# Performance work log

Measured on AMD Instinct MI355X. Metric: run time of the kernel, lower is better.

## Reference

```python
import jax, jax.numpy as jnp
import numpy as np

NUM_HEADS = 16
ROPE_BASE = 10000.0


def _rope(x):
    """Standard rotary embedding. x: (B, H, T, Dh), positions 0..T-1."""
    T, Dh = x.shape[-2], x.shape[-1]
    half = Dh // 2
    inv_freq = 1.0 / (ROPE_BASE ** (jnp.arange(half, dtype=jnp.float32) / half))
    ang = jnp.arange(T, dtype=jnp.float32)[:, None] * inv_freq[None, :]  # (T, half)
    cos, sin = jnp.cos(ang), jnp.sin(ang)
    x1, x2 = x[..., :half], x[..., half:]
    return jnp.concatenate([x1 * cos - x2 * sin, x1 * sin + x2 * cos], axis=-1)


def setup_inputs() -> dict:
    key = jax.random.key(0)
    ks = jax.random.split(key, 5)
    B, N, D = 8, 1025, 1024
    s = 1.0 / np.sqrt(D)
    return {
        "x": jax.random.normal(ks[0], (B, N, D), jnp.float32),
        "wq": jax.random.normal(ks[1], (D, D), jnp.float32) * s,
        "wk": jax.random.normal(ks[2], (D, D), jnp.float32) * s,
        "wv": jax.random.normal(ks[3], (D, D), jnp.float32) * s,
        "q_bias": jnp.zeros((D,), jnp.float32),
        "v_bias": jnp.zeros((D,), jnp.float32),
        "w_out": jax.random.normal(ks[4], (D, D), jnp.float32) * s,
        "b_out": jnp.zeros((D,), jnp.float32),
    }


def reference(x, wq, wk, wv, q_bias, v_bias, w_out, b_out):
    B, N, D = x.shape
    H = NUM_HEADS
    Dh = D // H
    scale = Dh ** -0.5

    q = x @ wq + q_bias           # (B, N, D)
    k = x @ wk
    v = x @ wv + v_bias

    def split_heads(t):  # (B, N, D) -> (B, H, N, Dh)
        return t.reshape(B, N, H, Dh).transpose(0, 2, 1, 3)

    q, k, v = split_heads(q), split_heads(k), split_heads(v)

    # RoPE on all tokens except the first (CLS)
    q = jnp.concatenate([q[:, :, :1, :], _rope(q[:, :, 1:, :])], axis=2)
    k = jnp.concatenate([k[:, :, :1, :], _rope(k[:, :, 1:, :])], axis=2)

    attn = jnp.einsum('bhqd,bhkd->bhqk', q * scale, k)
    attn = jax.nn.softmax(attn, axis=-1)
    out = jnp.einsum('bhqk,bhkd->bhqd', attn, v)  # (B, H, N, Dh)
    out = out.transpose(0, 2, 1, 3).reshape(B, N, D)
    return out @ w_out + b_out
```

## Files before the change

kernel.cpp:

```cpp
#include <hip/hip_runtime.h>

typedef unsigned short u16;
typedef __attribute__((ext_vector_type(8))) short  short8;
typedef __attribute__((ext_vector_type(8))) __bf16 bf16x8;
typedef __attribute__((ext_vector_type(4))) __bf16 bf16x4;
typedef __attribute__((ext_vector_type(4))) float  f32x4;

#define DEV __device__ __forceinline__

#define BATCH 8
#define SEQ   1025
#define DMODEL 1024
#define NHEAD 16
#define DH    64
#define MROWS (BATCH*SEQ)
#define VPAD  1152
#define KROWS 1088

DEV float bf2f(u16 u) { union { unsigned int i; float f; } v; v.i = ((unsigned int)u) << 16; return v.f; }
DEV u16 f2bf(float f) {
  union { float f; unsigned int i; } v; v.f = f;
  unsigned int x = v.i;
  return (u16)((x + 0x7fffu + ((x >> 16) & 1u)) >> 16);
}

DEV f32x4 mfma16(bf16x8 a, bf16x8 b, f32x4 c) {
  return __builtin_amdgcn_mfma_f32_16x16x32_bf16(a, b, c, 0, 0, 0);
}

DEV void gload_lds16(const void* g, void* s) {
  __builtin_amdgcn_global_load_lds(
      (const __attribute__((address_space(1))) void*)g,
      (__attribute__((address_space(3))) void*)s, 16, 0, 0);
}

DEV float exp2_fast(float x) { float r; asm("v_exp_f32 %0, %1" : "=v"(r) : "v"(x)); return r; }
DEV unsigned cvt_pk_bf16(float lo, float hi) {
  unsigned r;
  asm("v_cvt_pk_bf16_f32 %0, %1, %2" : "=v"(r) : "v"(lo), "v"(hi));
  return r;
}

#define QSCALE (0.125f * 1.44269504088896341f)

__global__ void prep_kernel(const float* __restrict__ x,
                            const float* __restrict__ wq, const float* __restrict__ wk,
                            const float* __restrict__ wv, const float* __restrict__ wo,
                            u16* __restrict__ x_bf, u16* __restrict__ wtqkv,
                            u16* __restrict__ wtout,
                            float* __restrict__ cost, float* __restrict__ sint) {
  __shared__ float tile[64][65];
  const int blk = blockIdx.x, tid = threadIdx.x;
  if (blk < 4100) {
    int i = blk * 256 + tid;
    if (i >= MROWS * 1024 / 8) return;
    const float4* p = (const float4*)x + (size_t)i * 2;
    float4 a = p[0], b = p[1];
    short8 o;
    o[0] = (short)f2bf(a.x); o[1] = (short)f2bf(a.y); o[2] = (short)f2bf(a.z); o[3] = (short)f2bf(a.w);
    o[4] = (short)f2bf(b.x); o[5] = (short)f2bf(b.y); o[6] = (short)f2bf(b.z); o[7] = (short)f2bf(b.w);
    *(short8*)(x_bf + (size_t)i * 8) = o;
  } else if (blk < 5124) {
    int wg = blk - 4100;
    int z = wg >> 8, rem = wg & 255;
    int kx = rem & 15, ny = rem >> 4;
    const float* src = (z == 0) ? wq : (z == 1) ? wk : (z == 2) ? wv : wo;
    int k0 = kx * 64, n0 = ny * 64;
    int c = tid & 63, rq = tid >> 6;
#pragma unroll
    for (int p = 0; p < 16; ++p) {
      int r = p * 4 + rq;
      tile[r][c] = src[(size_t)(k0 + r) * 1024 + n0 + c];
    }
    __syncthreads();
    u16* dst = (z < 3) ? (wtqkv + (size_t)z * 1024 * 1024) : wtout;
#pragma unroll
    for (int p = 0; p < 16; ++p) {
      int r = p * 4 + rq;
      dst[(size_t)(n0 + r) * 1024 + k0 + c] = f2bf(tile[c][r]);
    }
  } else {
    int i = (blk - 5124) * 256 + tid;
    if (i >= 1024 * 32) return;
    int pos = i >> 5, d = i & 31;
    float inv = powf(10000.0f, -(float)d / 32.0f);
    float ang = (float)pos * inv;
    cost[i] = cosf(ang);
    sint[i] = sinf(ang);
  }
}

#define FENCE(N) asm volatile("s_waitcnt vmcnt(" N ") lgkmcnt(0)\n\ts_barrier" ::: "memory")

DEV void stage_half(const u16* __restrict__ gpanel, long row0, int kcol,
                    char* dst, int wid, int lane) {
#pragma unroll
  for (int s = 0; s < 2; ++s) {
    int tt = wid * 64 + lane;
    int row = s * 128 + (tt >> 2), c2 = tt & 3;
    const u16* src = gpanel + (row0 + row) * 1024 + kcol + ((c2 ^ ((row >> 1) & 3)) << 3);
    gload_lds16(src, dst + s * 8192 + wid * 1024);
  }
}

DEV void quad(const char* sm, int buf, int kk, int mh, int wrow, int wcol,
              int l4, int l15, f32x4 (&acc)[8][4]) {
  const char* Ab = sm + buf * 65536 + kk * 16384;
  const char* Bb = sm + buf * 65536 + 32768 + kk * 16384;
  bf16x8 bfr[4];
#pragma unroll
  for (int n = 0; n < 4; ++n) {
    int r = wcol * 64 + n * 16 + l15;
    bfr[n] = *(const bf16x8*)(Bb + r * 64 + ((l4 << 4) ^ (((r >> 1) & 3) << 4)));
  }
  bf16x8 af[4];
#pragma unroll
  for (int m = 0; m < 4; ++m) {
    int r = wrow * 128 + (mh * 4 + m) * 16 + l15;
    af[m] = *(const bf16x8*)(Ab + r * 64 + ((l4 << 4) ^ (((r >> 1) & 3) << 4)));
  }
  __builtin_amdgcn_s_setprio(1);
#pragma unroll
  for (int m = 0; m < 4; ++m)
#pragma unroll
    for (int n = 0; n < 4; ++n)
      acc[mh * 4 + m][n] = mfma16(af[m], bfr[n], acc[mh * 4 + m][n]);
  __builtin_amdgcn_s_setprio(0);
}

__global__ __launch_bounds__(512, 2) void gemm256(const u16* __restrict__ A,
    const u16* __restrict__ Bw, u16* __restrict__ Cout) {
  __shared__ char smem[131072];
  int mt, nt;
  {
    int orig = blockIdx.x;
    int xcd = orig & 7;
    int f = (xcd < 4 ? xcd * 50 : 200 + (xcd - 4) * 49) + (orig >> 3);
    if (f < 384) { int sr = f / 48, rem = f % 48; nt = rem >> 2; mt = sr * 4 + (rem & 3); }
    else { mt = 32; nt = f - 384; }
  }
  const int t = threadIdx.x;
  const int wid = t >> 6, lane = t & 63;
  const int l4 = lane >> 4, l15 = lane & 15;
  const int wrow = wid >> 2, wcol = wid & 3;
  const long rowA0 = (long)mt * 256;
  const long rowB0 = (long)nt * 256;

  f32x4 acc[8][4];
#pragma unroll
  for (int m = 0; m < 8; ++m)
#pragma unroll
    for (int n = 0; n < 4; ++n) { f32x4 z = {0.f,0.f,0.f,0.f}; acc[m][n] = z; }

  stage_half(A,  rowA0, 0,  smem + 0,     wid, lane);
  stage_half(Bw, rowB0, 0,  smem + 32768, wid, lane);
  stage_half(A,  rowA0, 32, smem + 16384, wid, lane);
  stage_half(Bw, rowB0, 32, smem + 49152, wid, lane);

  for (int j = 0; j < 7; ++j) {
    const int cY = (2 * j + 1) * 64, cX = (2 * j + 2) * 64;
    FENCE("4"); stage_half(A,  rowA0, cY,      smem + 65536 + 0,     wid, lane); quad(smem, 0, 0, 0, wrow, wcol, l4, l15, acc);
    FENCE("6"); stage_half(Bw, rowB0, cY,      smem + 65536 + 32768, wid, lane); quad(smem, 0, 0, 1, wrow, wcol, l4, l15, acc);
    FENCE("4"); stage_half(A,  rowA0, cY + 32, smem + 65536 + 16384, wid, lane); quad(smem, 0, 1, 0, wrow, wcol, l4, l15, acc);
    FENCE("6"); stage_half(Bw, rowB0, cY + 32, smem + 65536 + 49152, wid, lane); quad(smem, 0, 1, 1, wrow, wcol, l4, l15, acc);
    FENCE("4"); stage_half(A,  rowA0, cX,      smem + 0,     wid, lane); quad(smem, 1, 0, 0, wrow, wcol, l4, l15, acc);
    FENCE("6"); stage_half(Bw, rowB0, cX,      smem + 32768, wid, lane); quad(smem, 1, 0, 1, wrow, wcol, l4, l15, acc);
    FENCE("4"); stage_half(A,  rowA0, cX + 32, smem + 16384, wid, lane); quad(smem, 1, 1, 0, wrow, wcol, l4, l15, acc);
    FENCE("6"); stage_half(Bw, rowB0, cX + 32, smem + 49152, wid, lane); quad(smem, 1, 1, 1, wrow, wcol, l4, l15, acc);
  }
  {
    const int cY = 15 * 64;
    FENCE("4"); stage_half(A,  rowA0, cY,      smem + 65536 + 0,     wid, lane); quad(smem, 0, 0, 0, wrow, wcol, l4, l15, acc);
    FENCE("6"); stage_half(Bw, rowB0, cY,      smem + 65536 + 32768, wid, lane); quad(smem, 0, 0, 1, wrow, wcol, l4, l15, acc);
    FENCE("4"); stage_half(A,  rowA0, cY + 32, smem + 65536 + 16384, wid, lane); quad(smem, 0, 1, 0, wrow, wcol, l4, l15, acc);
    FENCE("6"); stage_half(Bw, rowB0, cY + 32, smem + 65536 + 49152, wid, lane); quad(smem, 0, 1, 1, wrow, wcol, l4, l15, acc);
    FENCE("4"); quad(smem, 1, 0, 0, wrow, wcol, l4, l15, acc);
    FENCE("4"); quad(smem, 1, 0, 1, wrow, wcol, l4, l15, acc);
    FENCE("0"); quad(smem, 1, 1, 0, wrow, wcol, l4, l15, acc);
    FENCE("0"); quad(smem, 1, 1, 1, wrow, wcol, l4, l15, acc);
  }

#pragma unroll
  for (int m = 0; m < 8; ++m)
#pragma unroll
    for (int rg = 0; rg < 4; ++rg) {
      long row = rowA0 + wrow * 128 + m * 16 + l4 * 4 + rg;
      if (row >= MROWS) continue;
#pragma unroll
      for (int n = 0; n < 4; ++n) {
        long col = rowB0 + wcol * 64 + n * 16 + l15;
        Cout[row * 3072 + col] = f2bf(acc[m][n][rg]);
      }
    }
}

DEV void map_tiles(int f, int MT, int NT, int& mt, int& nt) {
  int body = (MT & ~7) * NT;
  if (f >= body) { int r = f - body; mt = (MT & ~7) + r / NT; nt = r % NT; }
  else { int sr = f / (8 * NT); int rem = f - sr * 8 * NT; nt = rem >> 3; mt = sr * 8 + (rem & 7); }
}

__global__ __launch_bounds__(256) void gemm_out(const u16* __restrict__ A,
    const u16* __restrict__ Bw, float* __restrict__ Cout, const float* __restrict__ bias) {
  __shared__ char smem[32768];
  int mt, nt;
  { int wg = blockIdx.x; int f = (wg & 7) * 65 + (wg >> 3); map_tiles(f, 65, 8, mt, nt); }
  const int t = threadIdx.x;
  const int wid = t >> 6, lane = t & 63;
  const int l4 = lane >> 4, l15 = lane & 15;
  const int wr = wid >> 1, wc = wid & 1;
  const long rowA0 = (long)mt * 128;
  const long rowB0 = (long)nt * 128;

  f32x4 acc[4][4];
#pragma unroll
  for (int m = 0; m < 4; ++m)
#pragma unroll
    for (int n = 0; n < 4; ++n) { f32x4 z = {0.f,0.f,0.f,0.f}; acc[m][n] = z; }

  const int srow = t >> 3;
  const int scol = (t & 7) * 8;

  for (int k0 = 0; k0 < 1024; k0 += 64) {
    __syncthreads();
#pragma unroll
    for (int i = 0; i < 4; ++i) {
      const u16* ga = A  + (rowA0 + i * 32 + srow) * 1024 + k0 + scol;
      gload_lds16(ga, smem + i * 4096 + wid * 1024);
      const u16* gb = Bw + (rowB0 + i * 32 + srow) * 1024 + k0 + scol;
      gload_lds16(gb, smem + 16384 + i * 4096 + wid * 1024);
    }
    __syncthreads();

    bf16x8 af[4][2], bfr[4][2];
#pragma unroll
    for (int m = 0; m < 4; ++m)
#pragma unroll
      for (int kk = 0; kk < 2; ++kk)
        af[m][kk] = *(const bf16x8*)(smem + (wr * 64 + m * 16 + l15) * 128 + kk * 64 + l4 * 16);
#pragma unroll
    for (int n = 0; n < 4; ++n)
#pragma unroll
      for (int kk = 0; kk < 2; ++kk)
        bfr[n][kk] = *(const bf16x8*)(smem + 16384 + (wc * 64 + n * 16 + l15) * 128 + kk * 64 + l4 * 16);

#pragma unroll
    for (int m = 0; m < 4; ++m)
#pragma unroll
      for (int n = 0; n < 4; ++n)
#pragma unroll
        for (int kk = 0; kk < 2; ++kk)
          acc[m][n] = mfma16(af[m][kk], bfr[n][kk], acc[m][n]);
  }

#pragma unroll
  for (int m = 0; m < 4; ++m)
#pragma unroll
    for (int rg = 0; rg < 4; ++rg) {
      long row = rowA0 + wr * 64 + m * 16 + l4 * 4 + rg;
      if (row >= MROWS) continue;
#pragma unroll
      for (int n = 0; n < 4; ++n) {
        long col = rowB0 + wc * 64 + n * 16 + l15;
        Cout[row * 1024 + col] = acc[m][n][rg] + bias[col];
      }
    }
}

__global__ void postqkv_kernel(const u16* __restrict__ cq, const float* __restrict__ qb,
                               const float* __restrict__ vb,
                               const float* __restrict__ cost, const float* __restrict__ sint,
                               u16* __restrict__ Qh, u16* __restrict__ Kh,
                               u16* __restrict__ VTh) {
  __shared__ float tile[64][65];
  const int blk = blockIdx.x, tid = threadIdx.x;
  if (blk < 513) {
    int idx = blk * 256 + tid;
    if (idx >= MROWS * NHEAD) return;
    int h = idx & 15, row = idx >> 4;
    int b = row / SEQ, n = row - b * SEQ;
    const u16* src = cq + (size_t)row * 3072 + h * 64;
    size_t dq = ((size_t)(b * 16 + h) * SEQ   + n) * 64;
    size_t dk = ((size_t)(b * 16 + h) * KROWS + n) * 64;
    bool dorope = (n > 0);
    const float* ct = cost + (size_t)(n - 1) * 32;
    const float* st = sint + (size_t)(n - 1) * 32;
#pragma unroll
    for (int i = 0; i < 4; ++i) {
      short8 qlo = *(const short8*)(src + i * 8);
      short8 qhi = *(const short8*)(src + 32 + i * 8);
      short8 klo = *(const short8*)(src + 1024 + i * 8);
      short8 khi = *(const short8*)(src + 1024 + 32 + i * 8);
      short8 oqlo, oqhi, oklo, okhi;
#pragma unroll
      for (int j = 0; j < 8; ++j) {
        int d = i * 8 + j;
        float q1 = bf2f((u16)qlo[j]) + qb[h * 64 + d];
        float q2 = bf2f((u16)qhi[j]) + qb[h * 64 + 32 + d];
        float k1 = bf2f((u16)klo[j]);
        float k2 = bf2f((u16)khi[j]);
        float c = dorope ? ct[d] : 1.0f;
        float s = dorope ? st[d] : 0.0f;
        oqlo[j] = (short)f2bf((q1 * c - q2 * s) * QSCALE);
        oqhi[j] = (short)f2bf((q1 * s + q2 * c) * QSCALE);
        oklo[j] = (short)f2bf(k1 * c - k2 * s);
        okhi[j] = (short)f2bf(k1 * s + k2 * c);
      }
      *(short8*)(Qh + dq + i * 8)      = oqlo;
      *(short8*)(Qh + dq + 32 + i * 8) = oqhi;
      *(short8*)(Kh + dk + i * 8)      = oklo;
      *(short8*)(Kh + dk + 32 + i * 8) = okhi;
    }
  } else {
    int wg = blk - 513;
    int bh = wg / 18, nx = wg - bh * 18;
    int b = bh >> 4, h = bh & 15;
    int n0 = nx * 64;
    int c = tid & 63, rq = tid >> 6;
#pragma unroll
    for (int p = 0; p < 16; ++p) {
      int r = p * 4 + rq;
      int n = n0 + r;
      float v = 0.f;
      if (n < SEQ) v = bf2f(cq[(size_t)(b * SEQ + n) * 3072 + 2048 + h * 64 + c]) + vb[h * 64 + c];
      tile[r][c] = v;
    }
    __syncthreads();
#pragma unroll
    for (int p = 0; p < 16; ++p) {
      int d = p * 4 + rq;
      VTh[((size_t)bh * 64 + d) * VPAD + n0 + c] = f2bf(tile[c][d]);
    }
  }
}

DEV void stage_rows(const u16* __restrict__ g, size_t strideElems, char* lbase,
                    int wid, int lane) {
#pragma unroll
  for (int s = 0; s < 2; ++s) {
    int off = s * 4096 + wid * 1024 + lane * 16;
    int r = off >> 7, cs = (off >> 4) & 7;
    const u16* src = g + (size_t)r * strideElems + ((cs ^ (r & 7)) << 3);
    gload_lds16(src, lbase + s * 4096 + wid * 1024);
  }
}

__global__ __launch_bounds__(256, 4) void attn128(const u16* __restrict__ Qh,
    const u16* __restrict__ Kh, const u16* __restrict__ VTh,
    u16* __restrict__ xattn) {
  __shared__ char lds[32768];
  const int wg = blockIdx.x;
  const int x = (wg & 7) * 144 + (wg >> 3);
  const int qt = x % 9, bh = x / 9;
  const int b = bh >> 4, h = bh & 15;
  const int t = threadIdx.x, w = t >> 6, lane = t & 63;
  const int l4 = lane >> 4, l15 = lane & 15;
  const u16* Qb = Qh + (size_t)bh * (SEQ * 64);
  const u16* Kb = Kh + (size_t)bh * (KROWS * 64);
  const u16* Vb = VTh + (size_t)bh * (64 * VPAD);
  const int q0 = qt * 128 + w * 32;

  bf16x8 aq[2][2];
#pragma unroll
  for (int m = 0; m < 2; ++m) {
    int qr = q0 + m * 16 + l15; if (qr > SEQ - 1) qr = SEQ - 1;
    aq[m][0] = *(const bf16x8*)(Qb + (size_t)qr * 64 + l4 * 8);
    aq[m][1] = *(const bf16x8*)(Qb + (size_t)qr * 64 + 32 + l4 * 8);
  }
  bf16x8 ones;
  { union { unsigned u[4]; bf16x8 v; } ou;
    ou.u[0] = ou.u[1] = ou.u[2] = ou.u[3] = 0x3F803F80u; ones = ou.v; }

  f32x4 o[2][4], osum[2];
  float mrow[2];
#pragma unroll
  for (int m = 0; m < 2; ++m) {
#pragma unroll
    for (int n = 0; n < 4; ++n) { f32x4 z = {0.f,0.f,0.f,0.f}; o[m][n] = z; }
    f32x4 z = {0.f,0.f,0.f,0.f}; osum[m] = z;
    mrow[m] = -1e30f;
  }

  stage_rows(Kb, 64, lds, w, lane);
  stage_rows(Vb, VPAD, lds + 16384, w, lane);
  asm volatile("s_waitcnt vmcnt(0)" ::: "memory");
  __syncthreads();

  int cur = 0;
  for (int kt = 0; kt < 17; ++kt) {
    const int kb = kt * 64;
    if (kt < 16) {
      stage_rows(Kb + (size_t)(kb + 64) * 64, 64, lds + (cur ^ 1) * 8192, w, lane);
      stage_rows(Vb + (kb + 64), VPAD, lds + 16384 + (cur ^ 1) * 8192, w, lane);
    }
    const char* Kl = lds + cur * 8192;
    const char* Vl = lds + 16384 + cur * 8192;

    f32x4 s[2][4];
#pragma unroll
    for (int tt = 0; tt < 4; ++tt) {
      const int kr = tt * 16 + l15;
      const char* kp = Kl + kr * 128;
      bf16x8 bk0 = *(const bf16x8*)(kp + ((l4       ^ (kr & 7)) << 4));
      bf16x8 bk1 = *(const bf16x8*)(kp + (((4 + l4) ^ (kr & 7)) << 4));
#pragma unroll
      for (int m = 0; m < 2; ++m) {
        f32x4 z = {0.f,0.f,0.f,0.f};
        z = mfma16(bk0, aq[m][0], z);
        z = mfma16(bk1, aq[m][1], z);
        s[m][tt] = z;
      }
    }

    if (kt == 16) {
#pragma unroll
      for (int m = 0; m < 2; ++m) {
        s[m][0][0] = (l4 == 0) ? s[m][0][0] : -1e30f;
        s[m][0][1] = -1e30f; s[m][0][2] = -1e30f; s[m][0][3] = -1e30f;
#pragma unroll
        for (int tt = 1; tt < 4; ++tt) {
          s[m][tt][0] = -1e30f; s[m][tt][1] = -1e30f; s[m][tt][2] = -1e30f; s[m][tt][3] = -1e30f;
        }
      }
    }

    float tmax[2];
#pragma unroll
    for (int m = 0; m < 2; ++m) {
      float a0 = fmaxf(fmaxf(s[m][0][0], s[m][0][1]), fmaxf(s[m][0][2], s[m][0][3]));
      float a1 = fmaxf(fmaxf(s[m][1][0], s[m][1][1]), fmaxf(s[m][1][2], s[m][1][3]));
      float a2 = fmaxf(fmaxf(s[m][2][0], s[m][2][1]), fmaxf(s[m][2][2], s[m][2][3]));
      float a3 = fmaxf(fmaxf(s[m][3][0], s[m][3][1]), fmaxf(s[m][3][2], s[m][3][3]));
      float tm = fmaxf(fmaxf(a0, a1), fmaxf(a2, a3));
      tm = fmaxf(tm, __shfl_xor(tm, 16));
      tm = fmaxf(tm, __shfl_xor(tm, 32));
      tmax[m] = tm;
    }

    int needR = (tmax[0] > mrow[0] + 8.0f) || (tmax[1] > mrow[1] + 8.0f);
    if (__any(needR)) {
#pragma unroll
      for (int m = 0; m < 2; ++m) {
        float mnew = fmaxf(mrow[m], tmax[m]);
        float alpha = exp2_fast(mrow[m] - mnew);
        mrow[m] = mnew;
        float al[4];
#pragma unroll
        for (int rg = 0; rg < 4; ++rg) al[rg] = __shfl(alpha, l4 * 4 + rg);
#pragma unroll
        for (int n = 0; n < 4; ++n)
#pragma unroll
          for (int rg = 0; rg < 4; ++rg) o[m][n][rg] *= al[rg];
#pragma unroll
        for (int rg = 0; rg < 4; ++rg) osum[m][rg] *= al[rg];
      }
    }

    unsigned pk[2][4][2];
#pragma unroll
    for (int m = 0; m < 2; ++m)
#pragma unroll
      for (int tt = 0; tt < 4; ++tt) {
        float p0 = exp2_fast(s[m][tt][0] - mrow[m]);
        float p1 = exp2_fast(s[m][tt][1] - mrow[m]);
        float p2 = exp2_fast(s[m][tt][2] - mrow[m]);
        float p3 = exp2_fast(s[m][tt][3] - mrow[m]);
        pk[m][tt][0] = cvt_pk_bf16(p0, p1);
        pk[m][tt][1] = cvt_pk_bf16(p2, p3);
      }

#pragma unroll
    for (int kk = 0; kk < 2; ++kk) {
      bf16x8 pa[2];
#pragma unroll
      for (int m = 0; m < 2; ++m) {
        union { unsigned u[4]; bf16x8 v; } pu;
        pu.u[0] = pk[m][2 * kk][0];
        pu.u[1] = pk[m][2 * kk][1];
        pu.u[2] = pk[m][2 * kk + 1][0];
        pu.u[3] = pk[m][2 * kk + 1][1];
        pa[m] = pu.v;
      }
      const int inner = (l4 & 1) * 8;
      const int c0 = kk * 4 + (l4 >> 1);
#pragma unroll
      for (int n = 0; n < 4; ++n) {
        const int vr = n * 16 + l15;
        const char* vp = Vl + vr * 128;
        union { bf16x4 h[2]; bf16x8 v; } bu;
        bu.h[0] = *(const bf16x4*)(vp + ((c0 ^ (vr & 7)) << 4) + inner);
        bu.h[1] = *(const bf16x4*)(vp + (((c0 + 2) ^ (vr & 7)) << 4) + inner);
#pragma unroll
        for (int m = 0; m < 2; ++m)
          o[m][n] = mfma16(pa[m], bu.v, o[m][n]);
      }
#pragma unroll
      for (int m = 0; m < 2; ++m)
        osum[m] = mfma16(pa[m], ones, osum[m]);
    }

    asm volatile("s_waitcnt vmcnt(0)" ::: "memory");
    __syncthreads();
    cur ^= 1;
  }

#pragma unroll
  for (int m = 0; m < 2; ++m)
#pragma unroll
    for (int n = 0; n < 4; ++n)
#pragma unroll
      for (int rg = 0; rg < 4; ++rg) {
        int qrow = q0 + m * 16 + l4 * 4 + rg;
        if (qrow < SEQ)
          xattn[(size_t)(b * SEQ + qrow) * 1024 + h * 64 + n * 16 + l15] =
              f2bf(o[m][n][rg] / osum[m][rg]);
      }
}


extern "C" void kernel_launch(void* const* d_in, const int* in_sizes, int n_in,
                              void* d_out, int out_size, void* d_ws, size_t ws_size,
                              hipStream_t stream) {
  const float* x      = (const float*)d_in[0];
  const float* wq     = (const float*)d_in[1];
  const float* wk     = (const float*)d_in[2];
  const float* wv     = (const float*)d_in[3];
  const float* q_bias = (const float*)d_in[4];
  const float* v_bias = (const float*)d_in[5];
  const float* w_out  = (const float*)d_in[6];
  const float* b_out  = (const float*)d_in[7];

  char* ws = (char*)d_ws;
  size_t off = 0;
  auto alc = [&](size_t bytes) { size_t r = off; off += (bytes + 255) & ~(size_t)255; return r; };

  u16*  x_bf  = (u16*)(ws + alc((size_t)MROWS * 1024 * 2));
  u16*  wtqkv = (u16*)(ws + alc((size_t)3072 * 1024 * 2));
  u16*  wtout = (u16*)(ws + alc((size_t)1024 * 1024 * 2));
  u16*  xattn = (u16*)(ws + alc((size_t)MROWS * 1024 * 2));
  u16*  cqkv  = (u16*)(ws + alc((size_t)8448 * 3072 * 2));
  u16*  Qhp   = (u16*)(ws + alc((size_t)128 * SEQ * 64 * 2));
  u16*  Khp   = (u16*)(ws + alc((size_t)128 * KROWS * 64 * 2));
  u16*  VThp  = (u16*)(ws + alc((size_t)128 * 64 * VPAD * 2));
  float* cost = (float*)(ws + alc((size_t)1024 * 32 * 4));
  float* sint = (float*)(ws + alc((size_t)1024 * 32 * 4));
  (void)ws_size; (void)in_sizes; (void)n_in; (void)out_size;

  prep_kernel<<<dim3(5252), 256, 0, stream>>>(x, wq, wk, wv, w_out,
                                              x_bf, wtqkv, wtout, cost, sint);
  gemm256<<<dim3(396), 512, 0, stream>>>(x_bf, wtqkv, cqkv);
  postqkv_kernel<<<dim3(513 + 2304), 256, 0, stream>>>(cqkv, q_bias, v_bias,
                                                       cost, sint, Qhp, Khp, VThp);
  attn128<<<dim3(1152), 256, 0, stream>>>(Qhp, Khp, VThp, xattn);
  gemm_out<<<dim3(520), 256, 0, stream>>>(xattn, wtout, (float*)d_out, b_out);
}
```

Before: 236.5 us.

## Shrink QKV GEMM tile to 256x128 with triple-buffered K pipeline

The QKV projection GEMM goes from 256x256 tiles with a 2-buffer, half-step staged schedule to 256x128 tiles. It uses a 3-slot ring of 32-wide K slices, and the grid doubles to 792 blocks. LDS drops from 128KB to 72KB and accumulators halve, so launch bounds allow 4 blocks per CU. The aim is better occupancy and load balance across CUs and a simpler prefetch pipeline. In exchange, each block reuses fewer loaded operands, which raises global and LDS traffic per flop.

```diff
diff --git a/kernel.cpp b/kernel.cpp
--- a/kernel.cpp
+++ b/kernel.cpp
@@ -92,99 +92,89 @@
 
 #define FENCE(N) asm volatile("s_waitcnt vmcnt(" N ") lgkmcnt(0)\n\ts_barrier" ::: "memory")
 
-DEV void stage_half(const u16* __restrict__ gpanel, long row0, int kcol,
-                    char* dst, int wid, int lane) {
+DEV void stage_tile(const u16* __restrict__ A, long rowA0,
+                    const u16* __restrict__ Bw, long rowB0, int kcol,
+                    char* slot, int wid, int lane) {
+  int tt = wid * 64 + lane;
+  int c2 = tt & 3;
 #pragma unroll
   for (int s = 0; s < 2; ++s) {
-    int tt = wid * 64 + lane;
-    int row = s * 128 + (tt >> 2), c2 = tt & 3;
-    const u16* src = gpanel + (row0 + row) * 1024 + kcol + ((c2 ^ ((row >> 1) & 3)) << 3);
-    gload_lds16(src, dst + s * 8192 + wid * 1024);
-  }
-}
-
-DEV void quad(const char* sm, int buf, int kk, int mh, int wrow, int wcol,
-              int l4, int l15, f32x4 (&acc)[8][4]) {
-  const char* Ab = sm + buf * 65536 + kk * 16384;
-  const char* Bb = sm + buf * 65536 + 32768 + kk * 16384;
-  bf16x8 bfr[4];
-#pragma unroll
-  for (int n = 0; n < 4; ++n) {
-    int r = wcol * 64 + n * 16 + l15;
-    bfr[n] = *(const bf16x8*)(Bb + r * 64 + ((l4 << 4) ^ (((r >> 1) & 3) << 4)));
-  }
-  bf16x8 af[4];
-#pragma unroll
-  for (int m = 0; m < 4; ++m) {
-    int r = wrow * 128 + (mh * 4 + m) * 16 + l15;
-    af[m] = *(const bf16x8*)(Ab + r * 64 + ((l4 << 4) ^ (((r >> 1) & 3) << 4)));
-  }
-  __builtin_amdgcn_s_setprio(1);
-#pragma unroll
-  for (int m = 0; m < 4; ++m)
-#pragma unroll
-    for (int n = 0; n < 4; ++n)
-      acc[mh * 4 + m][n] = mfma16(af[m], bfr[n], acc[mh * 4 + m][n]);
-  __builtin_amdgcn_s_setprio(0);
-}
-
-__global__ __launch_bounds__(512, 2) void gemm256(const u16* __restrict__ A,
+    int row = s * 128 + (tt >> 2);
+    const u16* src = A + (rowA0 + row) * 1024 + kcol + ((c2 ^ ((row >> 1) & 3)) << 3);
+    gload_lds16(src, slot + s * 8192 + wid * 1024);
+  }
+  {
+    int row = tt >> 2;
+    const u16* src = Bw + (rowB0 + row) * 1024 + kcol + ((c2 ^ ((row >> 1) & 3)) << 3);
+    gload_lds16(src, slot + 16384 + wid * 1024);
+  }
+}
+
+__global__ __launch_bounds__(512, 4) void gemm256(const u16* __restrict__ A,
     const u16* __restrict__ Bw, u16* __restrict__ Cout) {
-  __shared__ char smem[131072];
+  __shared__ char smem[73728];
   int mt, nt;
   {
     int orig = blockIdx.x;
-    int xcd = orig & 7;
-    int f = (xcd < 4 ? xcd * 50 : 200 + (xcd - 4) * 49) + (orig >> 3);
-    if (f < 384) { int sr = f / 48, rem = f % 48; nt = rem >> 2; mt = sr * 4 + (rem & 3); }
-    else { mt = 32; nt = f - 384; }
+    int f = (orig & 7) * 99 + (orig >> 3);
+    if (f < 768) { int sr = f / 96, rem = f % 96; nt = rem >> 2; mt = sr * 4 + (rem & 3); }
+    else { mt = 32; nt = f - 768; }
   }
   const int t = threadIdx.x;
   const int wid = t >> 6, lane = t & 63;
   const int l4 = lane >> 4, l15 = lane & 15;
-  const int wrow = wid >> 2, wcol = wid & 3;
+  const int wrow = wid >> 1, wcol = wid & 1;
   const long rowA0 = (long)mt * 256;
-  const long rowB0 = (long)nt * 256;
-
-  f32x4 acc[8][4];
-#pragma unroll
-  for (int m = 0; m < 8; ++m)
+  const long rowB0 = (long)nt * 128;
+
+  f32x4 acc[4][4];
+#pragma unroll
+  for (int m = 0; m < 4; ++m)
 #pragma unroll
     for (int n = 0; n < 4; ++n) { f32x4 z = {0.f,0.f,0.f,0.f}; acc[m][n] = z; }
 
-  stage_half(A,  rowA0, 0,  smem + 0,     wid, lane);
-  stage_half(Bw, rowB0, 0,  smem + 32768, wid, lane);
-  stage_half(A,  rowA0, 32, smem + 16384, wid, lane);
-  stage_half(Bw, rowB0, 32, smem + 49152, wid, lane);
-
-  for (int j = 0; j < 7; ++j) {
-    const int cY = (2 * j + 1) * 64, cX = (2 * j + 2) * 64;
-    FENCE("4"); stage_half(A,  rowA0, cY,      smem + 65536 + 0,     wid, lane); quad(smem, 0, 0, 0, wrow, wcol, l4, l15, acc);
-    FENCE("6"); stage_half(Bw, rowB0, cY,      smem + 65536 + 32768, wid, lane); quad(smem, 0, 0, 1, wrow, wcol, l4, l15, acc);
-    FENCE("4"); stage_half(A,  rowA0, cY + 32, smem + 65536 + 16384, wid, lane); quad(smem, 0, 1, 0, wrow, wcol, l4, l15, acc);
-    FENCE("6"); stage_half(Bw, rowB0, cY + 32, smem + 65536 + 49152, wid, lane); quad(smem, 0, 1, 1, wrow, wcol, l4, l15, acc);
-    FENCE("4"); stage_half(A,  rowA0, cX,      smem + 0,     wid, lane); quad(smem, 1, 0, 0, wrow, wcol, l4, l15, acc);
-    FENCE("6"); stage_half(Bw, rowB0, cX,      smem + 32768, wid, lane); quad(smem, 1, 0, 1, wrow, wcol, l4, l15, acc);
-    FENCE("4"); stage_half(A,  rowA0, cX + 32, smem + 16384, wid, lane); quad(smem, 1, 1, 0, wrow, wcol, l4, l15, acc);
-    FENCE("6"); stage_half(Bw, rowB0, cX + 32, smem + 49152, wid, lane); quad(smem, 1, 1, 1, wrow, wcol, l4, l15, acc);
-  }
-  {
-    const int cY = 15 * 64;
-    FENCE("4"); stage_half(A,  rowA0, cY,      smem + 65536 + 0,     wid, lane); quad(smem, 0, 0, 0, wrow, wcol, l4, l15, acc);
-    FENCE("6"); stage_half(Bw, rowB0, cY,      smem + 65536 + 32768, wid, lane); quad(smem, 0, 0, 1, wrow, wcol, l4, l15, acc);
-    FENCE("4"); stage_half(A,  rowA0, cY + 32, smem + 65536 + 16384, wid, lane); quad(smem, 0, 1, 0, wrow, wcol, l4, l15, acc);
-    FENCE("6"); stage_half(Bw, rowB0, cY + 32, smem + 65536 + 49152, wid, lane); quad(smem, 0, 1, 1, wrow, wcol, l4, l15, acc);
-    FENCE("4"); quad(smem, 1, 0, 0, wrow, wcol, l4, l15, acc);
-    FENCE("4"); quad(smem, 1, 0, 1, wrow, wcol, l4, l15, acc);
-    FENCE("0"); quad(smem, 1, 1, 0, wrow, wcol, l4, l15, acc);
-    FENCE("0"); quad(smem, 1, 1, 1, wrow, wcol, l4, l15, acc);
-  }
-
-#pragma unroll
-  for (int m = 0; m < 8; ++m)
+  stage_tile(A, rowA0, Bw, rowB0, 0,  smem,         wid, lane);
+  __builtin_amdgcn_sched_barrier(0);
+  stage_tile(A, rowA0, Bw, rowB0, 32, smem + 24576, wid, lane);
+  FENCE("3");
+
+  int cur = 0;
+  for (int j = 0; j < 32; ++j) {
+    if (j < 30) {
+      int nb = cur + 2; if (nb >= 3) nb -= 3;
+      stage_tile(A, rowA0, Bw, rowB0, (j + 2) * 32, smem + nb * 24576, wid, lane);
+    }
+    const char* slot = smem + cur * 24576;
+    bf16x8 bfr[4];
+#pragma unroll
+    for (int n = 0; n < 4; ++n) {
+      int r = wcol * 64 + n * 16 + l15;
+      bfr[n] = *(const bf16x8*)(slot + 16384 + r * 64 + ((l4 ^ ((r >> 1) & 3)) << 4));
+    }
+    bf16x8 af[4];
+#pragma unroll
+    for (int m = 0; m < 4; ++m) {
+      int r = wrow * 64 + m * 16 + l15;
+      af[m] = *(const bf16x8*)(slot + r * 64 + ((l4 ^ ((r >> 1) & 3)) << 4));
+    }
+    __builtin_amdgcn_s_setprio(1);
+#pragma unroll
+    for (int m = 0; m < 4; ++m)
+#pragma unroll
+      for (int n = 0; n < 4; ++n)
+        acc[m][n] = mfma16(af[m], bfr[n], acc[m][n]);
+    __builtin_amdgcn_s_setprio(0);
+
+    if (j < 30)       { FENCE("3"); }
+    else if (j == 30) { FENCE("0"); }
+    if (++cur == 3) cur = 0;
+  }
+
+#pragma unroll
+  for (int m = 0; m < 4; ++m)
 #pragma unroll
     for (int rg = 0; rg < 4; ++rg) {
-      long row = rowA0 + wrow * 128 + m * 16 + l4 * 4 + rg;
+      long row = rowA0 + wrow * 64 + m * 16 + l4 * 4 + rg;
       if (row >= MROWS) continue;
 #pragma unroll
       for (int n = 0; n < 4; ++n) {
@@ -548,7 +538,7 @@
 
   prep_kernel<<<dim3(5252), 256, 0, stream>>>(x, wq, wk, wv, w_out,
                                               x_bf, wtqkv, wtout, cost, sint);
-  gemm256<<<dim3(396), 512, 0, stream>>>(x_bf, wtqkv, cqkv);
+  gemm256<<<dim3(792), 512, 0, stream>>>(x_bf, wtqkv, cqkv);
   postqkv_kernel<<<dim3(513 + 2304), 256, 0, stream>>>(cqkv, q_bias, v_bias,
                                                        cost, sint, Qhp, Khp, VThp);
   attn128<<<dim3(1152), 256, 0, stream>>>(Qhp, Khp, VThp, xattn);
```

Result: no change. 241.1 us (+1.9%).
